# Kernel optimization log

Measured on AMD Instinct MI355X. Metric: run time of the kernel, lower is better.

## Reference

```python
import jax, jax.numpy as jnp
import numpy as np

D_MODEL = 1024
NUM_EXPERTS = 64
TOP_K = 2
TEMPERATURE = 1.0


def setup_inputs() -> dict:
    key = jax.random.key(0)
    k1, k2, k3, k4 = jax.random.split(key, 4)
    mh_output = jax.random.normal(k1, (8, 4096, D_MODEL), dtype=jnp.float32)
    noise = jax.random.normal(k2, (8, 4096, NUM_EXPERTS), dtype=jnp.float32)  # randn_like sample, externalized
    # nn.Linear weights: shape [out, in], init normal(0, 0.02); biases zero
    W_route = jax.random.normal(k3, (NUM_EXPERTS, D_MODEL), dtype=jnp.float32) * 0.02
    b_route = jnp.zeros((NUM_EXPERTS,), dtype=jnp.float32)
    W_noise = jax.random.normal(k4, (NUM_EXPERTS, D_MODEL), dtype=jnp.float32) * 0.02
    b_noise = jnp.zeros((NUM_EXPERTS,), dtype=jnp.float32)
    return {"mh_output": mh_output, "noise": noise, "W_route": W_route,
            "b_route": b_route, "W_noise": W_noise, "b_noise": b_noise}


def reference(mh_output, noise, W_route, b_route, W_noise, b_noise):
    # logits = topkroute_linear(mh_output); noise_logits = noise_linear(mh_output)
    logits = jnp.einsum('bsd,ed->bse', mh_output, W_route) + b_route
    noise_logits = jnp.einsum('bsd,ed->bse', mh_output, W_noise) + b_noise
    # noisy logits = logits + temperature * randn * softplus(noise_logits)
    noisy = logits + TEMPERATURE * noise * jax.nn.softplus(noise_logits)
    # top-k, scatter into -inf, softmax  ==  softmax over top-k values scattered into zeros
    top_vals, indices = jax.lax.top_k(noisy, TOP_K)          # [b, s, k]
    probs_k = jax.nn.softmax(top_vals, axis=-1)              # softmax(-inf elsewhere) -> 0 elsewhere
    one_hot = jax.nn.one_hot(indices, NUM_EXPERTS, dtype=noisy.dtype)  # [b, s, k, E]
    router_output = jnp.sum(one_hot * probs_k[..., None], axis=-2)     # [b, s, E]
    return router_output, indices
```

## Files before the change

kernel.cpp:

```cpp
#include <hip/hip_runtime.h>
#include <hip/hip_bf16.h>
#include <math.h>


#define T_TOKENS 32768
#define D_MODEL  1024
#define NE       64
#define NCOL     128
#define M_TILE   32
#define NCHUNK   32
#define CS_LD    68
#define OUT_IDX_BASE ((size_t)T_TOKENS * NE)
#define W_ELEMS  (NCOL * D_MODEL)

typedef short  bf16x8  __attribute__((ext_vector_type(8)));
typedef float  floatx4 __attribute__((ext_vector_type(4)));

__device__ __forceinline__ float softplus_f(float x) {
    return fmaxf(x, 0.f) + log1pf(expf(-fabsf(x)));
}

__device__ __forceinline__ void gload_lds16(const float* g, void* l) {
    __builtin_amdgcn_global_load_lds(
        (const __attribute__((address_space(1))) void*)g,
        (__attribute__((address_space(3))) void*)l, 16, 0, 0);
}

__device__ __forceinline__ void cvt8frag(const float4 a, const float4 b,
                                         bf16x8* hi, bf16x8* lo) {
    float v[8] = {a.x, a.y, a.z, a.w, b.x, b.y, b.z, b.w};
    int hw[4], lw[4];
    #pragma unroll
    for (int p = 0; p < 4; ++p) {
        float2 f2 = make_float2(v[2 * p], v[2 * p + 1]);
        __hip_bfloat162 h2 = __float22bfloat162_rn(f2);
        int u; __builtin_memcpy(&u, &h2, 4);
        float h0 = __uint_as_float(((unsigned)u) << 16);
        float h1 = __uint_as_float(((unsigned)u) & 0xFFFF0000u);
        float2 l2 = make_float2(v[2 * p] - h0, v[2 * p + 1] - h1);
        __hip_bfloat162 L2 = __float22bfloat162_rn(l2);
        int ul; __builtin_memcpy(&ul, &L2, 4);
        hw[p] = u; lw[p] = ul;
    }
    int4 hp = make_int4(hw[0], hw[1], hw[2], hw[3]);
    int4 lp = make_int4(lw[0], lw[1], lw[2], lw[3]);
    __builtin_memcpy(hi, &hp, 16);
    __builtin_memcpy(lo, &lp, 16);
}

__global__ __launch_bounds__(256) void prepack_w(
    const float* __restrict__ Wr, const float* __restrict__ Wn,
    short* __restrict__ Bh, short* __restrict__ Bl)
{
    int g   = blockIdx.x * 256 + threadIdx.x;
    int n   = g & 15;
    int kg  = (g >> 4) & 127;
    int t2  = g >> 11;
    int col = t2 * 16 + n;
    const float* src = (col < NE ? Wr + (size_t)col * D_MODEL
                                 : Wn + (size_t)(col - NE) * D_MODEL) + kg * 8;
    float4 a = *(const float4*)src;
    float4 b = *(const float4*)(src + 4);
    bf16x8 hi, lo;
    cvt8frag(a, b, &hi, &lo);
    *(bf16x8*)(Bh + (size_t)g * 8) = hi;
    *(bf16x8*)(Bl + (size_t)g * 8) = lo;
}

__global__ __launch_bounds__(256, 4) void router_mfma(
    const float* __restrict__ A,
    const float* __restrict__ noise,
    const float* __restrict__ br,
    const float* __restrict__ bn,
    const short* __restrict__ Bh,
    const short* __restrict__ Bl,
    float* __restrict__ out)
{
    __shared__ __align__(16) float Abuf[2][M_TILE * 32];
    __shared__ float Cs[M_TILE * CS_LD];
    __shared__ float s_p1[M_TILE], s_p2[M_TILE];
    __shared__ int   s_e1[M_TILE], s_e2[M_TILE];

    const int tid  = threadIdx.x;
    const int lane = tid & 63;
    const int wid  = tid >> 6;
    const int n16  = lane & 15;
    const int quad = lane >> 4;
    const int m0   = blockIdx.x * M_TILE;

    const int srow = (wid << 3) + (lane >> 3);
    const int schk = (lane & 7) ^ (lane >> 3);
    const float* gA = A + (size_t)(m0 + srow) * D_MODEL + schk * 4;
    float* lb0 = &Abuf[0][wid * 256];
    float* lb1 = &Abuf[1][wid * 256];

    const int bBaseR = ((wid * 128 + quad) * 16 + n16) * 8;
    const int bBaseN = (((wid + 4) * 128 + quad) * 16 + n16) * 8;

    int rdOff[2][2];
    #pragma unroll
    for (int mf = 0; mf < 2; ++mf) {
        int r  = mf * 16 + n16;
        int s0 = (2 * quad)     ^ (n16 & 7);
        int s1 = (2 * quad + 1) ^ (n16 & 7);
        rdOff[mf][0] = r * 32 + s0 * 4;
        rdOff[mf][1] = r * 32 + s1 * 4;
    }

    floatx4 accR[2], accN[2];
    #pragma unroll
    for (int mf = 0; mf < 2; ++mf) { accR[mf] = (floatx4)0.f; accN[mf] = (floatx4)0.f; }

    gload_lds16(gA, lb0);
    __syncthreads();

    for (int kc = 0; kc < NCHUNK; ++kc) {
        const int cur = kc & 1;

        if (kc + 1 < NCHUNK)
            gload_lds16(gA + (kc + 1) * 32, (cur ? lb0 : lb1));

        const int o = kc * 512;
        bf16x8 bhR = *(const bf16x8*)(Bh + bBaseR + o);
        bf16x8 blR = *(const bf16x8*)(Bl + bBaseR + o);
        bf16x8 bhN = *(const bf16x8*)(Bh + bBaseN + o);
        bf16x8 blN = *(const bf16x8*)(Bl + bBaseN + o);

        bf16x8 ah[2], al[2];
        #pragma unroll
        for (int mf = 0; mf < 2; ++mf) {
            float4 f0 = *(const float4*)&Abuf[cur][rdOff[mf][0]];
            float4 f1 = *(const float4*)&Abuf[cur][rdOff[mf][1]];
            cvt8frag(f0, f1, &ah[mf], &al[mf]);
        }

        #pragma unroll
        for (int mf = 0; mf < 2; ++mf) {
            accR[mf] = __builtin_amdgcn_mfma_f32_16x16x32_bf16(ah[mf], bhR, accR[mf], 0, 0, 0);
            accR[mf] = __builtin_amdgcn_mfma_f32_16x16x32_bf16(ah[mf], blR, accR[mf], 0, 0, 0);
            accR[mf] = __builtin_amdgcn_mfma_f32_16x16x32_bf16(al[mf], bhR, accR[mf], 0, 0, 0);
            accN[mf] = __builtin_amdgcn_mfma_f32_16x16x32_bf16(ah[mf], bhN, accN[mf], 0, 0, 0);
            accN[mf] = __builtin_amdgcn_mfma_f32_16x16x32_bf16(ah[mf], blN, accN[mf], 0, 0, 0);
            accN[mf] = __builtin_amdgcn_mfma_f32_16x16x32_bf16(al[mf], bhN, accN[mf], 0, 0, 0);
        }

        __syncthreads();
    }

    {
        int e = wid * 16 + n16;
        float brv = br[e], bnv = bn[e];
        #pragma unroll
        for (int mf = 0; mf < 2; ++mf)
            #pragma unroll
            for (int rr = 0; rr < 4; ++rr) {
                int t = mf * 16 + quad * 4 + rr;
                float nz    = noise[(size_t)(m0 + t) * NE + e];
                float route = accR[mf][rr] + brv;
                float nl    = accN[mf][rr] + bnv;
                Cs[t * CS_LD + e] = fmaf(nz, softplus_f(nl), route);
            }
    }
    __syncthreads();

    if (tid < M_TILE) {
        const int t = tid;
        float v1 = -INFINITY, v2 = -INFINITY;
        int e1 = 0, e2 = 0;
        #pragma unroll
        for (int e4 = 0; e4 < 16; ++e4) {
            float4 q = *(const float4*)&Cs[t * CS_LD + e4 * 4];
            float qa[4] = {q.x, q.y, q.z, q.w};
            #pragma unroll
            for (int c = 0; c < 4; ++c) {
                float v = qa[c];
                int e = e4 * 4 + c;
                if (v > v1) { v2 = v1; e2 = e1; v1 = v; e1 = e; }
                else if (v > v2) { v2 = v; e2 = e; }
            }
        }
        float ex = expf(v2 - v1);
        float denom = 1.f + ex;
        s_p1[t] = 1.f / denom;
        s_p2[t] = ex / denom;
        s_e1[t] = e1;
        s_e2[t] = e2;
        float2 iv = make_float2((float)e1, (float)e2);
        *(float2*)(out + OUT_IDX_BASE + (size_t)(m0 + t) * 2) = iv;
    }
    __syncthreads();

    #pragma unroll
    for (int i = 0; i < 2; ++i) {
        int gi = i * 256 + tid;
        int t  = gi >> 4;
        int e0 = (gi & 15) * 4;
        float p1 = s_p1[t], p2 = s_p2[t];
        int   e1 = s_e1[t], e2 = s_e2[t];
        float4 v;
        v.x = (e0 + 0 == e1) ? p1 : ((e0 + 0 == e2) ? p2 : 0.f);
        v.y = (e0 + 1 == e1) ? p1 : ((e0 + 1 == e2) ? p2 : 0.f);
        v.z = (e0 + 2 == e1) ? p1 : ((e0 + 2 == e2) ? p2 : 0.f);
        v.w = (e0 + 3 == e1) ? p1 : ((e0 + 3 == e2) ? p2 : 0.f);
        *(float4*)(out + (size_t)(m0 + t) * NE + e0) = v;
    }
}

extern "C" void kernel_launch(void* const* d_in, const int* in_sizes, int n_in,
                              void* d_out, int out_size, void* d_ws, size_t ws_size,
                              hipStream_t stream) {
    const float* A     = (const float*)d_in[0];
    const float* noise = (const float*)d_in[1];
    const float* Wr    = (const float*)d_in[2];
    const float* br    = (const float*)d_in[3];
    const float* Wn    = (const float*)d_in[4];
    const float* bn    = (const float*)d_in[5];
    float* out = (float*)d_out;

    short* Bh = (short*)d_ws;
    short* Bl = Bh + W_ELEMS;

    prepack_w<<<dim3(W_ELEMS / 8 / 256), dim3(256), 0, stream>>>(Wr, Wn, Bh, Bl);
    router_mfma<<<dim3(T_TOKENS / M_TILE), dim3(256), 0, stream>>>(A, noise, br, bn, Bh, Bl, out);
}
```

Before: 234.2 us.

## Enlarge token tile to 128 and stage prepacked weights through LDS

Raises the token tile from 32 to 128 rows and the block from 256 to 512 threads arranged as a 4x2 wave grid. Each wave now computes a 32x32 sub-tile, and the prepacked bf16 hi/lo weight fragments are double-buffered into LDS alongside A. The aim is to reuse each weight chunk across more tokens, cutting global weight traffic per token and raising MFMA work per load. In exchange LDS use per block grows, the grid shrinks to 256 blocks, and only 128 threads do the top-2 scan in the epilogue.

```diff
diff --git a/kernel.cpp b/kernel.cpp
--- a/kernel.cpp
+++ b/kernel.cpp
@@ -7,7 +7,7 @@
 #define D_MODEL  1024
 #define NE       64
 #define NCOL     128
-#define M_TILE   32
+#define M_TILE   128
 #define NCHUNK   32
 #define CS_LD    68
 #define OUT_IDX_BASE ((size_t)T_TOKENS * NE)
@@ -20,7 +20,7 @@
     return fmaxf(x, 0.f) + log1pf(expf(-fabsf(x)));
 }
 
-__device__ __forceinline__ void gload_lds16(const float* g, void* l) {
+__device__ __forceinline__ void gload_lds16(const void* g, void* l) {
     __builtin_amdgcn_global_load_lds(
         (const __attribute__((address_space(1))) void*)g,
         (__attribute__((address_space(3))) void*)l, 16, 0, 0);
@@ -67,7 +67,7 @@
     *(bf16x8*)(Bl + (size_t)g * 8) = lo;
 }
 
-__global__ __launch_bounds__(256, 4) void router_mfma(
+__global__ __launch_bounds__(512, 1) void router_mfma(
     const float* __restrict__ A,
     const float* __restrict__ noise,
     const float* __restrict__ br,
@@ -76,7 +76,8 @@
     const short* __restrict__ Bl,
     float* __restrict__ out)
 {
-    __shared__ __align__(16) float Abuf[2][M_TILE * 32];
+    __shared__ __align__(16) float Abuf[2][4096];
+    __shared__ __align__(16) short Bbuf[2][8192];
     __shared__ float Cs[M_TILE * CS_LD];
     __shared__ float s_p1[M_TILE], s_p2[M_TILE];
     __shared__ int   s_e1[M_TILE], s_e2[M_TILE];
@@ -84,80 +85,88 @@
     const int tid  = threadIdx.x;
     const int lane = tid & 63;
     const int wid  = tid >> 6;
+    const int wm   = wid >> 1;
+    const int wn   = wid & 1;
     const int n16  = lane & 15;
     const int quad = lane >> 4;
     const int m0   = blockIdx.x * M_TILE;
 
-    const int srow = (wid << 3) + (lane >> 3);
-    const int schk = (lane & 7) ^ (lane >> 3);
-    const float* gA = A + (size_t)(m0 + srow) * D_MODEL + schk * 4;
-    float* lb0 = &Abuf[0][wid * 256];
-    float* lb1 = &Abuf[1][wid * 256];
-
-    const int bBaseR = ((wid * 128 + quad) * 16 + n16) * 8;
-    const int bBaseN = (((wid + 4) * 128 + quad) * 16 + n16) * 8;
-
-    int rdOff[2][2];
-    #pragma unroll
-    for (int mf = 0; mf < 2; ++mf) {
-        int r  = mf * 16 + n16;
-        int s0 = (2 * quad)     ^ (n16 & 7);
-        int s1 = (2 * quad + 1) ^ (n16 & 7);
-        rdOff[mf][0] = r * 32 + s0 * 4;
-        rdOff[mf][1] = r * 32 + s1 * 4;
-    }
-
-    floatx4 accR[2], accN[2];
-    #pragma unroll
-    for (int mf = 0; mf < 2; ++mf) { accR[mf] = (floatx4)0.f; accN[mf] = (floatx4)0.f; }
-
-    gload_lds16(gA, lb0);
+    const float* gAst = A + (size_t)(m0 + wid * 16 + n16) * D_MODEL + quad * 8;
+    const int   sp  = wid >> 2;
+    const int   st0 = (wid & 3) * 2;
+    const short* gBst = (sp ? Bl : Bh) + (size_t)lane * 8;
+
+    floatx4 accR[2][2], accN[2][2];
+    #pragma unroll
+    for (int mf = 0; mf < 2; ++mf)
+        #pragma unroll
+        for (int fi = 0; fi < 2; ++fi) { accR[mf][fi] = (floatx4)0.f; accN[mf][fi] = (floatx4)0.f; }
+
+    gload_lds16(gAst + 0, &Abuf[0][(wid * 2 + 0) * 256]);
+    gload_lds16(gAst + 4, &Abuf[0][(wid * 2 + 1) * 256]);
+    gload_lds16(gBst + (size_t)st0 * 16384,       &Bbuf[0][(sp * 8 + st0) * 512]);
+    gload_lds16(gBst + (size_t)(st0 + 1) * 16384, &Bbuf[0][(sp * 8 + st0 + 1) * 512]);
     __syncthreads();
 
     for (int kc = 0; kc < NCHUNK; ++kc) {
-        const int cur = kc & 1;
-
-        if (kc + 1 < NCHUNK)
-            gload_lds16(gA + (kc + 1) * 32, (cur ? lb0 : lb1));
-
-        const int o = kc * 512;
-        bf16x8 bhR = *(const bf16x8*)(Bh + bBaseR + o);
-        bf16x8 blR = *(const bf16x8*)(Bl + bBaseR + o);
-        bf16x8 bhN = *(const bf16x8*)(Bh + bBaseN + o);
-        bf16x8 blN = *(const bf16x8*)(Bl + bBaseN + o);
+        const int cur = kc & 1, nxt = cur ^ 1;
+
+        if (kc + 1 < NCHUNK) {
+            const int ka = (kc + 1) * 32;
+            const int kb = (kc + 1) * 512;
+            gload_lds16(gAst + ka,     &Abuf[nxt][(wid * 2 + 0) * 256]);
+            gload_lds16(gAst + ka + 4, &Abuf[nxt][(wid * 2 + 1) * 256]);
+            gload_lds16(gBst + (size_t)st0 * 16384 + kb,       &Bbuf[nxt][(sp * 8 + st0) * 512]);
+            gload_lds16(gBst + (size_t)(st0 + 1) * 16384 + kb, &Bbuf[nxt][(sp * 8 + st0 + 1) * 512]);
+        }
 
         bf16x8 ah[2], al[2];
         #pragma unroll
         for (int mf = 0; mf < 2; ++mf) {
-            float4 f0 = *(const float4*)&Abuf[cur][rdOff[mf][0]];
-            float4 f1 = *(const float4*)&Abuf[cur][rdOff[mf][1]];
+            const int r16 = wm * 2 + mf;
+            float4 f0 = *(const float4*)&Abuf[cur][(r16 * 2 + 0) * 256 + lane * 4];
+            float4 f1 = *(const float4*)&Abuf[cur][(r16 * 2 + 1) * 256 + lane * 4];
             cvt8frag(f0, f1, &ah[mf], &al[mf]);
         }
 
-        #pragma unroll
-        for (int mf = 0; mf < 2; ++mf) {
-            accR[mf] = __builtin_amdgcn_mfma_f32_16x16x32_bf16(ah[mf], bhR, accR[mf], 0, 0, 0);
-            accR[mf] = __builtin_amdgcn_mfma_f32_16x16x32_bf16(ah[mf], blR, accR[mf], 0, 0, 0);
-            accR[mf] = __builtin_amdgcn_mfma_f32_16x16x32_bf16(al[mf], bhR, accR[mf], 0, 0, 0);
-            accN[mf] = __builtin_amdgcn_mfma_f32_16x16x32_bf16(ah[mf], bhN, accN[mf], 0, 0, 0);
-            accN[mf] = __builtin_amdgcn_mfma_f32_16x16x32_bf16(ah[mf], blN, accN[mf], 0, 0, 0);
-            accN[mf] = __builtin_amdgcn_mfma_f32_16x16x32_bf16(al[mf], bhN, accN[mf], 0, 0, 0);
-        }
+        bf16x8 bhR[2], blR[2], bhN[2], blN[2];
+        #pragma unroll
+        for (int fi = 0; fi < 2; ++fi) {
+            const int tR = 2 * wn + fi;
+            const int tN = 4 + 2 * wn + fi;
+            bhR[fi] = *(const bf16x8*)&Bbuf[cur][(0 * 8 + tR) * 512 + lane * 8];
+            blR[fi] = *(const bf16x8*)&Bbuf[cur][(1 * 8 + tR) * 512 + lane * 8];
+            bhN[fi] = *(const bf16x8*)&Bbuf[cur][(0 * 8 + tN) * 512 + lane * 8];
+            blN[fi] = *(const bf16x8*)&Bbuf[cur][(1 * 8 + tN) * 512 + lane * 8];
+        }
+
+        #pragma unroll
+        for (int mf = 0; mf < 2; ++mf)
+            #pragma unroll
+            for (int fi = 0; fi < 2; ++fi) {
+                accR[mf][fi] = __builtin_amdgcn_mfma_f32_16x16x32_bf16(ah[mf], bhR[fi], accR[mf][fi], 0, 0, 0);
+                accR[mf][fi] = __builtin_amdgcn_mfma_f32_16x16x32_bf16(ah[mf], blR[fi], accR[mf][fi], 0, 0, 0);
+                accR[mf][fi] = __builtin_amdgcn_mfma_f32_16x16x32_bf16(al[mf], bhR[fi], accR[mf][fi], 0, 0, 0);
+                accN[mf][fi] = __builtin_amdgcn_mfma_f32_16x16x32_bf16(ah[mf], bhN[fi], accN[mf][fi], 0, 0, 0);
+                accN[mf][fi] = __builtin_amdgcn_mfma_f32_16x16x32_bf16(ah[mf], blN[fi], accN[mf][fi], 0, 0, 0);
+                accN[mf][fi] = __builtin_amdgcn_mfma_f32_16x16x32_bf16(al[mf], bhN[fi], accN[mf][fi], 0, 0, 0);
+            }
 
         __syncthreads();
     }
 
-    {
-        int e = wid * 16 + n16;
+    #pragma unroll
+    for (int fi = 0; fi < 2; ++fi) {
+        const int e = wn * 32 + fi * 16 + n16;
         float brv = br[e], bnv = bn[e];
         #pragma unroll
         for (int mf = 0; mf < 2; ++mf)
             #pragma unroll
             for (int rr = 0; rr < 4; ++rr) {
-                int t = mf * 16 + quad * 4 + rr;
+                const int t = wm * 32 + mf * 16 + quad * 4 + rr;
                 float nz    = noise[(size_t)(m0 + t) * NE + e];
-                float route = accR[mf][rr] + brv;
-                float nl    = accN[mf][rr] + bnv;
+                float route = accR[mf][fi][rr] + brv;
+                float nl    = accN[mf][fi][rr] + bnv;
                 Cs[t * CS_LD + e] = fmaf(nz, softplus_f(nl), route);
             }
     }
@@ -191,8 +200,8 @@
     __syncthreads();
 
     #pragma unroll
-    for (int i = 0; i < 2; ++i) {
-        int gi = i * 256 + tid;
+    for (int i = 0; i < 4; ++i) {
+        int gi = i * 512 + tid;
         int t  = gi >> 4;
         int e0 = (gi & 15) * 4;
         float p1 = s_p1[t], p2 = s_p2[t];
@@ -221,5 +230,5 @@
     short* Bl = Bh + W_ELEMS;
 
     prepack_w<<<dim3(W_ELEMS / 8 / 256), dim3(256), 0, stream>>>(Wr, Wn, Bh, Bl);
-    router_mfma<<<dim3(T_TOKENS / M_TILE), dim3(256), 0, stream>>>(A, noise, br, bn, Bh, Bl, out);
-}
+    router_mfma<<<dim3(T_TOKENS / M_TILE), dim3(512), 0, stream>>>(A, noise, br, bn, Bh, Bl, out);
+}
```

Measured after the change: 240.3 us. 2.6% more time.
